# Kernel optimization log

Measured on AMD Instinct MI355X. Metric: run time of the kernel, lower is better.

The kernel has to match this reference:

```python
import jax, jax.numpy as jnp
import numpy as np

TAU = 0.8
V_TH = 0.5
W_D1_GPI = -0.8
W_D2_STN = 0.5
W_STN_GPI = 0.6
GPI_TONIC = 0.4
NOISE = 0.1
T, B = 512, 256
N_D1, N_D2, N_GPI, N_STN = 128, 128, 64, 64


def setup_inputs() -> dict:
    key = jax.random.key(0)
    ks = jax.random.split(key, 7)
    return {
        "x": jax.random.normal(ks[0], (T, B, 2), dtype=jnp.float32),
        "dopa": jax.random.uniform(ks[1], (T, B), dtype=jnp.float32),
        "rpe": jax.random.normal(ks[2], (T, B), dtype=jnp.float32),
        "W_d1": jax.random.normal(ks[3], (N_D1, 2), dtype=jnp.float32) * 0.5,
        "W_d2": jax.random.normal(ks[4], (N_D2, 2), dtype=jnp.float32) * 0.5,
        "noise_d1": jax.random.normal(ks[5], (T, B, N_D1), dtype=jnp.float32),
        "noise_d2": jax.random.normal(ks[6], (T, B, N_D2), dtype=jnp.float32),
    }


def reference(x, dopa, rpe, W_d1, W_d2, noise_d1, noise_d2):
    """Runs T LIF steps of the spiking basal-ganglia circuit for B circuits.

    Returns gates [T, B] = d1_rate - gpi_rate per step. rpe is unused (as in source).
    """
    dt = x.dtype
    v0 = (
        jnp.zeros((B, N_D1), dt),
        jnp.zeros((B, N_D2), dt),
        jnp.zeros((B, N_GPI), dt),
        jnp.zeros((B, N_STN), dt),
    )

    def lif(v, I):
        v = TAU * v + (1.0 - TAU) * I
        s = (v >= V_TH).astype(dt)
        return v * (1.0 - s), s

    def step(carry, inp):
        v_d1, v_d2, v_gpi, v_stn = carry
        xt, dop, nd1, nd2 = inp  # [B,2], [B], [B,N], [B,N]
        d1_mod = (1.0 + dop * 0.5)[:, None]
        d2_mod = (1.0 - dop * 0.3)[:, None]
        I_d1 = jnp.einsum("bi,ni->bn", xt, W_d1) * d1_mod
        v_d1, s_d1 = lif(v_d1, I_d1 + nd1 * NOISE)
        I_d2 = jnp.einsum("bi,ni->bn", xt, W_d2) * d2_mod
        v_d2, s_d2 = lif(v_d2, I_d2 + nd2 * NOISE)
        I_stn = (s_d2.mean(axis=1) * W_D2_STN)[:, None]  # [B,1] broadcast to [B,N_STN]
        v_stn, s_stn = lif(v_stn, I_stn)
        I_gpi = (GPI_TONIC + s_d1.mean(axis=1) * W_D1_GPI + s_stn.mean(axis=1) * W_STN_GPI)[:, None]
        v_gpi, s_gpi = lif(v_gpi, I_gpi)
        gate = s_d1.mean(axis=1) - s_gpi.mean(axis=1)  # [B]
        return (v_d1, v_d2, v_gpi, v_stn), gate

    _, gates = jax.lax.scan(step, v0, (x, dopa, noise_d1, noise_d2))
    return gates  # [T, B]
```

## Files before the change

### kernel.cpp

```cpp
#include <hip/hip_runtime.h>


__global__ __launch_bounds__(576, 1) void bg_kernel(
    const float* __restrict__ x,
    const float* __restrict__ dopa,
    const float* __restrict__ Wd1,
    const float* __restrict__ Wd2,
    const float* __restrict__ nd1,
    const float* __restrict__ nd2,
    float* __restrict__ out)
{
#pragma clang fp contract(off)
    constexpr int T = 512, B = 256;
    constexpr int S = 32;
    constexpr int NCH = T / S;
    constexpr size_t TSTRIDE = (size_t)B * 128;

    __shared__ float lds_I[3][S][64][4];
    __shared__ float lds_x[T][2];
    __shared__ float lds_d[T];

    const int b    = blockIdx.x;
    const int tid  = threadIdx.x;
    const int wv   = tid >> 6;
    const int lane = tid & 63;

    for (int t = tid; t < T; t += 576) {
        const float2 xv = *(const float2*)(x + (size_t)t * (B * 2) + b * 2);
        lds_x[t][0] = xv.x;
        lds_x[t][1] = xv.y;
        lds_d[t]    = dopa[(size_t)t * B + b];
    }
    __syncthreads();

    if (wv == 0) {
        __syncthreads();

        float v1a = 0.0f, v1b = 0.0f;
        float v2a = 0.0f, v2b = 0.0f;
        float v_stn = 0.0f, v_gpi = 0.0f;
        float gate_reg = 0.0f;

        for (int i = 0; i < NCH; ++i) {
            const float (*buf)[64][4] = lds_I[i % 3];

#pragma unroll
            for (int s = 0; s < S; ++s) {
                const float4 I = *(const float4*)&buf[s][lane][0];

                v1a = 0.8f * v1a + 0.2f * I.x;
                v1b = 0.8f * v1b + 0.2f * I.y;
                v2a = 0.8f * v2a + 0.2f * I.z;
                v2b = 0.8f * v2b + 0.2f * I.w;

                const bool s1a = v1a >= 0.5f, s1b = v1b >= 0.5f;
                const bool s2a = v2a >= 0.5f, s2b = v2b >= 0.5f;
                v1a = s1a ? 0.0f : v1a;
                v1b = s1b ? 0.0f : v1b;
                v2a = s2a ? 0.0f : v2a;
                v2b = s2b ? 0.0f : v2b;

                const int c1 = __popcll(__ballot(s1a)) + __popcll(__ballot(s1b));
                const int c2 = __popcll(__ballot(s2a)) + __popcll(__ballot(s2b));
                const float mean1 = (float)c1 * 0.0078125f;
                const float mean2 = (float)c2 * 0.0078125f;

                const float I_stn = mean2 * 0.5f;
                v_stn = 0.8f * v_stn + 0.2f * I_stn;
                const float s_stn = (v_stn >= 0.5f) ? 1.0f : 0.0f;
                v_stn = (v_stn >= 0.5f) ? 0.0f : v_stn;

                const float I_gpi = (0.4f + mean1 * -0.8f) + s_stn * 0.6f;
                v_gpi = 0.8f * v_gpi + 0.2f * I_gpi;
                const float s_gpi = (v_gpi >= 0.5f) ? 1.0f : 0.0f;
                v_gpi = (v_gpi >= 0.5f) ? 0.0f : v_gpi;

                const float gate = mean1 - s_gpi;

                const int latch = ((i & 1) << 5) | s;
                gate_reg = (lane == latch) ? gate : gate_reg;
            }

            if (i & 1) {
                const int t0 = (i - 1) * S;
                out[(size_t)(t0 + lane) * B + b] = gate_reg;
            }

            __syncthreads();
        }
    } else {
        const float4 w1 = *(const float4*)(Wd1 + 4 * lane);
        const float4 w2 = *(const float4*)(Wd2 + 4 * lane);
        const float* n1b = nd1 + (size_t)b * 128 + 2 * lane;
        const float* n2b = nd2 + (size_t)b * 128 + 2 * lane;
        const int p0 = (wv - 1) * 4;

        auto stage = [&](int c, int bf) {
            const int tbase = c * S;
            float2 a1[4], a2[4];
#pragma unroll
            for (int j = 0; j < 4; ++j) {
                const int t = tbase + p0 + j;
                a1[j] = *(const float2*)(n1b + (size_t)t * TSTRIDE);
                a2[j] = *(const float2*)(n2b + (size_t)t * TSTRIDE);
            }
#pragma unroll
            for (int j = 0; j < 4; ++j) {
                const int s = p0 + j;
                const int t = tbase + s;
                const float xx = lds_x[t][0], xy = lds_x[t][1];
                const float dop = lds_d[t];

                const float m1 = 1.0f + dop * 0.5f;
                const float m2 = 1.0f - dop * 0.3f;

                const float dot1a = __builtin_fmaf(xy, w1.y, xx * w1.x);
                const float dot1b = __builtin_fmaf(xy, w1.w, xx * w1.z);
                const float dot2a = __builtin_fmaf(xy, w2.y, xx * w2.x);
                const float dot2b = __builtin_fmaf(xy, w2.w, xx * w2.z);

                float4 I;
                I.x = dot1a * m1 + a1[j].x * 0.1f;
                I.y = dot1b * m1 + a1[j].y * 0.1f;
                I.z = dot2a * m2 + a2[j].x * 0.1f;
                I.w = dot2b * m2 + a2[j].y * 0.1f;

                *(float4*)&lds_I[bf][s][lane][0] = I;
            }
        };

        stage(0, 0);
        stage(1, 1);
        __syncthreads();

        for (int i = 0; i < NCH; ++i) {
            if (i + 2 < NCH) stage(i + 2, (i + 2) % 3);
            __syncthreads();
        }
    }
}

extern "C" void kernel_launch(void* const* d_in, const int* in_sizes, int n_in,
                              void* d_out, int out_size, void* d_ws, size_t ws_size,
                              hipStream_t stream) {
    const float* x    = (const float*)d_in[0];
    const float* dopa = (const float*)d_in[1];
    const float* Wd1  = (const float*)d_in[3];
    const float* Wd2  = (const float*)d_in[4];
    const float* nd1  = (const float*)d_in[5];
    const float* nd2  = (const float*)d_in[6];
    float* out = (float*)d_out;

    bg_kernel<<<dim3(256), dim3(576), 0, stream>>>(x, dopa, Wd1, Wd2, nd1, nd2, out);
}
```

Measured before the change: 192.7 us.

## Split D1/D2 recurrences across four waves, then run STN/GPi scan afterward

The kernel moves from a producer/consumer scheme (8 waves staging currents through a triple LDS buffer, 1 wave running all LIF updates) to 4 waves that each own 64 neurons of D1 or D2. Each wave runs its own voltage recurrence over all T steps, prefetching noise into registers 16 steps ahead. It writes per-step spike counts to LDS, and a final single-wave pass runs the scalar STN/GPi recurrence using shuffles. This removes the per-chunk block barriers and the serial 4-neuron-per-lane critical path. In exchange it relies on register double-buffering for memory latency and adds a serial tail pass.

```diff
diff --git a/kernel.cpp b/kernel.cpp
--- a/kernel.cpp
+++ b/kernel.cpp
@@ -1,7 +1,7 @@
 #include <hip/hip_runtime.h>
 
 
-__global__ __launch_bounds__(576, 1) void bg_kernel(
+__global__ __launch_bounds__(256, 1) void bg_kernel(
     const float* __restrict__ x,
     const float* __restrict__ dopa,
     const float* __restrict__ Wd1,
@@ -12,58 +12,90 @@
 {
 #pragma clang fp contract(off)
     constexpr int T = 512, B = 256;
-    constexpr int S = 32;
-    constexpr int NCH = T / S;
     constexpr size_t TSTRIDE = (size_t)B * 128;
 
-    __shared__ float lds_I[3][S][64][4];
-    __shared__ float lds_x[T][2];
-    __shared__ float lds_d[T];
+    __shared__ float lds_xm[T][4];
+    __shared__ uint4 cnt_lds[T];
 
     const int b    = blockIdx.x;
     const int tid  = threadIdx.x;
     const int wv   = tid >> 6;
     const int lane = tid & 63;
+    const int pop  = wv >> 1;
+    const int half = wv & 1;
 
-    for (int t = tid; t < T; t += 576) {
+    for (int t = tid; t < T; t += 256) {
         const float2 xv = *(const float2*)(x + (size_t)t * (B * 2) + b * 2);
-        lds_x[t][0] = xv.x;
-        lds_x[t][1] = xv.y;
-        lds_d[t]    = dopa[(size_t)t * B + b];
+        const float dop = dopa[(size_t)t * B + b];
+        lds_xm[t][0] = xv.x;
+        lds_xm[t][1] = xv.y;
+        lds_xm[t][2] = 1.0f + dop * 0.5f;
+        lds_xm[t][3] = 1.0f - dop * 0.3f;
     }
     __syncthreads();
 
+    {
+        const int n = half * 64 + lane;
+        const float* nb = (pop ? nd2 : nd1) + (size_t)b * 128 + n;
+        const float2 w  = *(const float2*)((pop ? Wd2 : Wd1) + 2 * n);
+
+        float va = 0.0f;
+        unsigned int cnt_reg = 0u;
+
+        float arrA[16], arrB[16];
+
+#define LOADG(dst, t0)                                                       \
+        { _Pragma("unroll")                                                  \
+          for (int k = 0; k < 16; ++k)                                       \
+              dst[k] = nb[(size_t)((t0) + k) * TSTRIDE]; }
+
+#define PROCG(src, t0, lbase)                                                \
+        { _Pragma("unroll")                                                  \
+          for (int k = 0; k < 16; ++k) {                                     \
+              const float4 xm = *(const float4*)&lds_xm[(t0) + k][0];        \
+              const float m   = pop ? xm.w : xm.z;                           \
+              const float dot = __builtin_fmaf(xm.y, w.y, xm.x * w.x);       \
+              const float I   = dot * m + src[k] * 0.1f;                     \
+              va = 0.8f * va + 0.2f * I;                                     \
+              const bool s = va >= 0.5f;                                     \
+              va = s ? 0.0f : va;                                            \
+              const int c = __popcll(__ballot(s));                           \
+              cnt_reg = (lane == (lbase) + k) ? (unsigned int)c : cnt_reg;   \
+          } }
+
+        LOADG(arrA, 0)
+        LOADG(arrB, 16)
+        for (int gp = 0; gp < 16; ++gp) {
+            const int t0 = gp * 32;
+            const int lb = (gp & 1) * 32;
+            PROCG(arrA, t0, lb)
+            if (gp < 15) LOADG(arrA, t0 + 32)
+            PROCG(arrB, t0 + 16, lb + 16)
+            if (gp < 15) LOADG(arrB, t0 + 48)
+            if (gp & 1) {
+                const int tw = (gp - 1) * 32;
+                ((unsigned int*)&cnt_lds[tw + lane])[wv] = cnt_reg;
+            }
+        }
+#undef LOADG
+#undef PROCG
+    }
+
+    __syncthreads();
+
     if (wv == 0) {
-        __syncthreads();
+        float v_stn = 0.0f, v_gpi = 0.0f;
 
-        float v1a = 0.0f, v1b = 0.0f;
-        float v2a = 0.0f, v2b = 0.0f;
-        float v_stn = 0.0f, v_gpi = 0.0f;
-        float gate_reg = 0.0f;
+        for (int g = 0; g < 8; ++g) {
+            const uint4 c4 = cnt_lds[g * 64 + lane];
+            const float mean1v = (float)(int)(c4.x + c4.y) * 0.0078125f;
+            const float mean2v = (float)(int)(c4.z + c4.w) * 0.0078125f;
 
-        for (int i = 0; i < NCH; ++i) {
-            const float (*buf)[64][4] = lds_I[i % 3];
-
+            float gate_reg = 0.0f;
 #pragma unroll
-            for (int s = 0; s < S; ++s) {
-                const float4 I = *(const float4*)&buf[s][lane][0];
-
-                v1a = 0.8f * v1a + 0.2f * I.x;
-                v1b = 0.8f * v1b + 0.2f * I.y;
-                v2a = 0.8f * v2a + 0.2f * I.z;
-                v2b = 0.8f * v2b + 0.2f * I.w;
-
-                const bool s1a = v1a >= 0.5f, s1b = v1b >= 0.5f;
-                const bool s2a = v2a >= 0.5f, s2b = v2b >= 0.5f;
-                v1a = s1a ? 0.0f : v1a;
-                v1b = s1b ? 0.0f : v1b;
-                v2a = s2a ? 0.0f : v2a;
-                v2b = s2b ? 0.0f : v2b;
-
-                const int c1 = __popcll(__ballot(s1a)) + __popcll(__ballot(s1b));
-                const int c2 = __popcll(__ballot(s2a)) + __popcll(__ballot(s2b));
-                const float mean1 = (float)c1 * 0.0078125f;
-                const float mean2 = (float)c2 * 0.0078125f;
+            for (int j = 0; j < 64; ++j) {
+                const float mean1 = __shfl(mean1v, j);
+                const float mean2 = __shfl(mean2v, j);
 
                 const float I_stn = mean2 * 0.5f;
                 v_stn = 0.8f * v_stn + 0.2f * I_stn;
@@ -77,65 +109,9 @@
 
                 const float gate = mean1 - s_gpi;
 
-                const int latch = ((i & 1) << 5) | s;
-                gate_reg = (lane == latch) ? gate : gate_reg;
+                gate_reg = (lane == j) ? gate : gate_reg;
             }
-
-            if (i & 1) {
-                const int t0 = (i - 1) * S;
-                out[(size_t)(t0 + lane) * B + b] = gate_reg;
-            }
-
-            __syncthreads();
-        }
-    } else {
-        const float4 w1 = *(const float4*)(Wd1 + 4 * lane);
-        const float4 w2 = *(const float4*)(Wd2 + 4 * lane);
-        const float* n1b = nd1 + (size_t)b * 128 + 2 * lane;
-        const float* n2b = nd2 + (size_t)b * 128 + 2 * lane;
-        const int p0 = (wv - 1) * 4;
-
-        auto stage = [&](int c, int bf) {
-            const int tbase = c * S;
-            float2 a1[4], a2[4];
-#pragma unroll
-            for (int j = 0; j < 4; ++j) {
-                const int t = tbase + p0 + j;
-                a1[j] = *(const float2*)(n1b + (size_t)t * TSTRIDE);
-                a2[j] = *(const float2*)(n2b + (size_t)t * TSTRIDE);
-            }
-#pragma unroll
-            for (int j = 0; j < 4; ++j) {
-                const int s = p0 + j;
-                const int t = tbase + s;
-                const float xx = lds_x[t][0], xy = lds_x[t][1];
-                const float dop = lds_d[t];
-
-                const float m1 = 1.0f + dop * 0.5f;
-                const float m2 = 1.0f - dop * 0.3f;
-
-                const float dot1a = __builtin_fmaf(xy, w1.y, xx * w1.x);
-                const float dot1b = __builtin_fmaf(xy, w1.w, xx * w1.z);
-                const float dot2a = __builtin_fmaf(xy, w2.y, xx * w2.x);
-                const float dot2b = __builtin_fmaf(xy, w2.w, xx * w2.z);
-
-                float4 I;
-                I.x = dot1a * m1 + a1[j].x * 0.1f;
-                I.y = dot1b * m1 + a1[j].y * 0.1f;
-                I.z = dot2a * m2 + a2[j].x * 0.1f;
-                I.w = dot2b * m2 + a2[j].y * 0.1f;
-
-                *(float4*)&lds_I[bf][s][lane][0] = I;
-            }
-        };
-
-        stage(0, 0);
-        stage(1, 1);
-        __syncthreads();
-
-        for (int i = 0; i < NCH; ++i) {
-            if (i + 2 < NCH) stage(i + 2, (i + 2) % 3);
-            __syncthreads();
+            out[(size_t)(g * 64 + lane) * B + b] = gate_reg;
         }
     }
 }
@@ -151,5 +127,5 @@
     const float* nd2  = (const float*)d_in[6];
     float* out = (float*)d_out;
 
-    bg_kernel<<<dim3(256), dim3(576), 0, stream>>>(x, dopa, Wd1, Wd2, nd1, nd2, out);
+    bg_kernel<<<dim3(256), dim3(256), 0, stream>>>(x, dopa, Wd1, Wd2, nd1, nd2, out);
 }
```

New measurement: 186.8 us. 3.1% less time.
